# Kernel optimization log

Hardware: AMD Instinct MI355X
Metric: run time of the kernel (lower is better)

## Reference

```python
import jax, jax.numpy as jnp
import numpy as np

STRIDES = (8, 16, 32, 64, 128)
HS = (192, 96, 48, 24, 12)
NUM_CLASSES = 15
NUM_THETA = 18
B = 16
SCORE_THR = 0.05
IOU_THR = 0.3
MAX_DET = 1000


def setup_inputs() -> dict:
    key = jax.random.key(0)
    ks = jax.random.split(key, 20)
    inp = {}
    i = 0
    for name, c in (("cls", NUM_CLASSES), ("reg", 5), ("tc", NUM_THETA), ("tr", 1)):
        for l, h in enumerate(HS):
            inp[f"{name}_l{l}"] = jax.random.normal(ks[i], (B, c, h, h), dtype=jnp.float32)
            i += 1
    return inp


def _coords():
    # FCOS-style location centers per level, concatenated: [N, 2] (x, y)
    outs = []
    for h, s in zip(HS, STRIDES):
        c1d = jnp.arange(h, dtype=jnp.float32) * s + s // 2
        yy, xx = jnp.meshgrid(c1d, c1d, indexing="ij")
        outs.append(jnp.stack([xx.ravel(), yy.ravel()], axis=-1))
    return jnp.concatenate(outs, axis=0)


def _flatten(levels):
    # list of [B,C,h,w] -> [B, sum(h*w), C]  (permute to NHWC then reshape, as in torch)
    b = levels[0].shape[0]
    return jnp.concatenate(
        [jnp.transpose(t, (0, 2, 3, 1)).reshape(b, -1, t.shape[1]) for t in levels], axis=1
    )


def _pairwise_iou(boxes):
    # boxes [M,5] (x1,y1,x2,y2,theta); axis-aligned IoU on first 4 coords
    x1, y1, x2, y2 = boxes[:, 0], boxes[:, 1], boxes[:, 2], boxes[:, 3]
    area = jnp.clip(x2 - x1, 0.0) * jnp.clip(y2 - y1, 0.0)
    iw = jnp.clip(jnp.minimum(x2[:, None], x2[None, :]) - jnp.maximum(x1[:, None], x1[None, :]), 0.0)
    ih = jnp.clip(jnp.minimum(y2[:, None], y2[None, :]) - jnp.maximum(y1[:, None], y1[None, :]), 0.0)
    inter = iw * ih
    union = area[:, None] + area[None, :] - inter
    return inter / jnp.maximum(union, 1e-8)


def _nms_keep(boxes, valid, iou_thr):
    # greedy NMS over score-sorted boxes; returns bool keep mask [M]
    m = boxes.shape[0]
    iou = _pairwise_iou(boxes)
    idx = jnp.arange(m)

    def body(i, keep):
        sup = keep[i] & (iou[i] > iou_thr) & (idx > i)
        return keep & ~sup

    return jax.lax.fori_loop(0, m, body, valid)


def _forward(cls_levels, reg_levels, tc_levels, tr_levels):
    coords = _coords()  # [N,2]

    cls_preds = jax.nn.sigmoid(_flatten(cls_levels))          # [B,N,15]
    cls_scores = jnp.max(cls_preds, axis=-1)                   # [B,N]
    cls_classes = jnp.argmax(cls_preds, axis=-1) + 1           # [B,N]

    tc_preds = jax.nn.sigmoid(_flatten(tc_levels))             # [B,N,18]
    theta_c = (jnp.argmax(tc_preds, axis=-1) + 1)[..., None].astype(jnp.float32)  # [B,N,1]
    tr_lo = _flatten(tr_levels)                                # [B,N,1]
    theta = theta_c * 10.0 + tr_lo                             # [B,N,1]

    # reg: scale ltrb channels (0:4) by stride per level, keep angle channel raw
    reg_parts = []
    for t, s in zip(reg_levels, STRIDES):
        r = jnp.transpose(t, (0, 2, 3, 1)).reshape(t.shape[0], -1, 5)
        reg_parts.append(jnp.concatenate([r[..., :4] * float(s), r[..., 4:]], axis=-1))
    reg = jnp.concatenate(reg_parts, axis=1)                   # [B,N,5]

    x1y1 = coords[None, :, :] - reg[..., :2]
    x2y2 = coords[None, :, :] + reg[..., 2:4]
    boxes = jnp.concatenate([x1y1, x2y2, theta], axis=-1)      # [B,N,5]

    max_num = min(MAX_DET, cls_scores.shape[-1])
    top_scores, top_idx = jax.lax.top_k(cls_scores, max_num)   # sorted desc
    boxes_topk = jnp.take_along_axis(boxes, top_idx[..., None], axis=1)   # [B,M,5]
    classes_topk = jnp.take_along_axis(cls_classes, top_idx, axis=1)      # [B,M]

    valid = top_scores >= SCORE_THR
    keep = jax.vmap(lambda b, v: _nms_keep(b, v, IOU_THR))(boxes_topk, valid)  # [B,M] bool

    scores_post = top_scores * keep
    classes_post = classes_topk * keep
    boxes_post = boxes_topk * keep[..., None]
    return scores_post, classes_post, boxes_post


def reference(cls_l0, cls_l1, cls_l2, cls_l3, cls_l4,
              reg_l0, reg_l1, reg_l2, reg_l3, reg_l4,
              tc_l0, tc_l1, tc_l2, tc_l3, tc_l4,
              tr_l0, tr_l1, tr_l2, tr_l3, tr_l4):
    return _forward(
        [cls_l0, cls_l1, cls_l2, cls_l3, cls_l4],
        [reg_l0, reg_l1, reg_l2, reg_l3, reg_l4],
        [tc_l0, tc_l1, tc_l2, tc_l3, tc_l4],
        [tr_l0, tr_l1, tr_l2, tr_l3, tr_l4],
    )
```

## Files before the change

kernel.cpp:

```cpp
#include <hip/hip_runtime.h>
#include <stdint.h>

#define NCLS   15
#define NTH    18
#define BATCH  16
#define NANCH  49104
#define KTOP   1000
#define NWORDS 16
#define NBIN   32768
#define BSHIFT 15
#define CAND   2048

__device__ __forceinline__ float sigmoidf(float x) {
    return 1.0f / (1.0f + expf(-x));
}

__device__ __forceinline__ void levelOf(int i, int& lvl, int& h, int& s, int& pos) {
    if (i < 36864)      { lvl = 0; h = 192; s = 8;   pos = i; }
    else if (i < 46080) { lvl = 1; h = 96;  s = 16;  pos = i - 36864; }
    else if (i < 48384) { lvl = 2; h = 48;  s = 32;  pos = i - 46080; }
    else if (i < 48960) { lvl = 3; h = 24;  s = 64;  pos = i - 48384; }
    else                { lvl = 4; h = 12;  s = 128; pos = i - 48960; }
}

__device__ __forceinline__ unsigned long long shfl_u64(unsigned long long v, int src) {
    int lo = __shfl((int)(unsigned int)(v & 0xFFFFFFFFull), src);
    int hi = __shfl((int)(unsigned int)(v >> 32), src);
    return ((unsigned long long)(unsigned int)hi << 32) | (unsigned long long)(unsigned int)lo;
}

__device__ __forceinline__ void atomicOr64Shared(unsigned long long* p, unsigned long long v) {
    unsigned int* q = (unsigned int*)p;
    unsigned int lo = (unsigned int)v;
    unsigned int hi = (unsigned int)(v >> 32);
    if (lo) atomicOr(q, lo);
    if (hi) atomicOr(q + 1, hi);
}

__global__ __launch_bounds__(256) void k_zero(uint4* __restrict__ p, int n4)
{
    int i = blockIdx.x * 256 + threadIdx.x;
    if (i < n4) p[i] = make_uint4(0u, 0u, 0u, 0u);
}

__global__ __launch_bounds__(256) void k_scores(
    const float* __restrict__ c0, const float* __restrict__ c1,
    const float* __restrict__ c2, const float* __restrict__ c3,
    const float* __restrict__ c4,
    float* __restrict__ scores, unsigned int* __restrict__ hist)
{
    __shared__ unsigned int lh[NBIN / 2];
    const int b = blockIdx.y;
    for (int i = threadIdx.x; i < NBIN / 2; i += 256) lh[i] = 0u;
    __syncthreads();

    #pragma unroll
    for (int r = 0; r < 2; ++r) {
        int f4 = blockIdx.x * 512 + r * 256 + threadIdx.x;
        if (f4 < NANCH / 4) {
            int i = f4 * 4;
            int lvl, h, s, pos;
            levelOf(i, lvl, h, s, pos);
            int hh = h * h;
            const float* cp = (lvl == 0) ? c0 : (lvl == 1) ? c1 : (lvl == 2) ? c2
                              : (lvl == 3) ? c3 : c4;
            const float* base = cp + (size_t)b * NCLS * hh + pos;
            float4 mx = make_float4(-1e30f, -1e30f, -1e30f, -1e30f);
            #pragma unroll
            for (int c = 0; c < NCLS; ++c) {
                float4 v = *(const float4*)(base + (size_t)c * hh);
                mx.x = fmaxf(mx.x, v.x); mx.y = fmaxf(mx.y, v.y);
                mx.z = fmaxf(mx.z, v.z); mx.w = fmaxf(mx.w, v.w);
            }
            float4 sc = make_float4(sigmoidf(mx.x), sigmoidf(mx.y),
                                    sigmoidf(mx.z), sigmoidf(mx.w));
            *(float4*)(scores + (size_t)b * NANCH + i) = sc;
            unsigned int bin;
            bin = __float_as_uint(sc.x) >> BSHIFT;
            atomicAdd(&lh[bin >> 1], 1u << ((bin & 1) << 4));
            bin = __float_as_uint(sc.y) >> BSHIFT;
            atomicAdd(&lh[bin >> 1], 1u << ((bin & 1) << 4));
            bin = __float_as_uint(sc.z) >> BSHIFT;
            atomicAdd(&lh[bin >> 1], 1u << ((bin & 1) << 4));
            bin = __float_as_uint(sc.w) >> BSHIFT;
            atomicAdd(&lh[bin >> 1], 1u << ((bin & 1) << 4));
        }
    }
    __syncthreads();

    unsigned int* hb = hist + (size_t)b * NBIN;
    for (int wd = threadIdx.x; wd < NBIN / 2; wd += 256) {
        unsigned int v = lh[wd];
        if (v) {
            unsigned int lo = v & 0xFFFFu, hi = v >> 16;
            if (lo) atomicAdd(&hb[wd * 2], lo);
            if (hi) atomicAdd(&hb[wd * 2 + 1], hi);
        }
    }
}

__global__ __launch_bounds__(256) void k_findT(
    const unsigned int* __restrict__ hist, int* __restrict__ tbin)
{
    int b = blockIdx.x;
    int tid = threadIdx.x;
    const unsigned int* hb = hist + (size_t)b * NBIN;
    __shared__ unsigned int sc[256];
    __shared__ unsigned int fsc[128];
    __shared__ int s_c, s_t;

    unsigned int s = 0;
    const uint4* hv = (const uint4*)(hb + (size_t)tid * 128);
    #pragma unroll 8
    for (int k = 0; k < 32; ++k) {
        uint4 v = hv[k];
        s += v.x + v.y + v.z + v.w;
    }
    sc[tid] = s;
    if (tid == 0) { s_c = 0; s_t = 0; }
    __syncthreads();
    for (int d = 1; d < 256; d <<= 1) {
        unsigned int add = (tid + d < 256) ? sc[tid + d] : 0;
        __syncthreads();
        sc[tid] += add;
        __syncthreads();
    }
    if (sc[tid] >= (unsigned int)KTOP && (tid == 255 || sc[tid + 1] < (unsigned int)KTOP))
        s_c = tid;
    __syncthreads();
    int c = s_c;
    unsigned int hi = (c < 255) ? sc[c + 1] : 0;
    if (tid < 128) fsc[tid] = hb[c * 128 + tid];
    __syncthreads();
    for (int d = 1; d < 128; d <<= 1) {
        unsigned int add = (tid < 128 && tid + d < 128) ? fsc[tid + d] : 0;
        __syncthreads();
        if (tid < 128) fsc[tid] += add;
        __syncthreads();
    }
    if (tid < 128 && hi + fsc[tid] >= (unsigned int)KTOP &&
        (tid == 127 || hi + fsc[tid + 1] < (unsigned int)KTOP))
        s_t = tid;
    __syncthreads();
    if (tid == 0) tbin[b] = c * 128 + s_t;
}

__global__ __launch_bounds__(256) void k_compact(
    const float* __restrict__ scores, const int* __restrict__ tbin,
    int* __restrict__ cnt, unsigned long long* __restrict__ cand)
{
    const int b = blockIdx.y;
    const int t4 = blockIdx.x * 256 + threadIdx.x;
    __shared__ int lcnt;
    __shared__ int lbase;
    if (threadIdx.x == 0) lcnt = 0;
    __syncthreads();

    const int T = tbin[b];
    const bool in = (t4 < NANCH / 4);
    float4 v = make_float4(0.f, 0.f, 0.f, 0.f);
    if (in) v = *(const float4*)(scores + (size_t)b * NANCH + 4 * (size_t)t4);
    unsigned int bits[4] = { __float_as_uint(v.x), __float_as_uint(v.y),
                             __float_as_uint(v.z), __float_as_uint(v.w) };
    int rank[4];
    #pragma unroll
    for (int k = 0; k < 4; ++k) {
        bool pass = in && ((int)(bits[k] >> BSHIFT) >= T);
        rank[k] = pass ? atomicAdd(&lcnt, 1) : -1;
    }
    __syncthreads();
    if (threadIdx.x == 0) lbase = atomicAdd(&cnt[b * 16], lcnt);
    __syncthreads();
    const int base = lbase;
    #pragma unroll
    for (int k = 0; k < 4; ++k) {
        if (rank[k] >= 0) {
            int p = base + rank[k];
            if (p < CAND) {
                unsigned int idx = 4u * (unsigned int)t4 + (unsigned int)k;
                cand[(size_t)b * CAND + p] =
                    ((unsigned long long)bits[k] << 32) |
                    (unsigned long long)(0xFFFFFFFFu - idx);
            }
        }
    }
}

__global__ __launch_bounds__(1024) void k_sortk(
    const unsigned long long* __restrict__ cand, const int* __restrict__ cnt,
    float* __restrict__ tsc, int* __restrict__ tix)
{
    int b = blockIdx.x;
    int tid = threadIdx.x;
    __shared__ unsigned long long keys[CAND];
    int n = cnt[b * 16]; if (n > CAND) n = CAND;
    for (int i = tid; i < CAND; i += 1024)
        keys[i] = (i < n) ? cand[(size_t)b * CAND + i] : 0ull;
    __syncthreads();
    for (int sz = 2; sz <= CAND; sz <<= 1) {
        for (int st = sz >> 1; st > 0; st >>= 1) {
            for (int i = tid; i < CAND; i += 1024) {
                int j = i ^ st;
                if (j > i) {
                    unsigned long long a = keys[i], c = keys[j];
                    bool desc = ((i & sz) == 0);
                    if (desc ? (a < c) : (a > c)) { keys[i] = c; keys[j] = a; }
                }
            }
            __syncthreads();
        }
    }
    if (tid < KTOP) {
        unsigned long long key = keys[tid];
        tsc[b * KTOP + tid] = __uint_as_float((unsigned int)(key >> 32));
        tix[b * KTOP + tid] = (int)(0xFFFFFFFFu - (unsigned int)(key & 0xFFFFFFFFull));
    }
}

__global__ __launch_bounds__(256) void k_decode(
    const float* __restrict__ c0, const float* __restrict__ c1,
    const float* __restrict__ c2, const float* __restrict__ c3,
    const float* __restrict__ c4,
    const float* __restrict__ r0, const float* __restrict__ r1,
    const float* __restrict__ r2, const float* __restrict__ r3,
    const float* __restrict__ r4,
    const float* __restrict__ t0, const float* __restrict__ t1,
    const float* __restrict__ t2, const float* __restrict__ t3,
    const float* __restrict__ t4,
    const float* __restrict__ q0, const float* __restrict__ q1,
    const float* __restrict__ q2, const float* __restrict__ q3,
    const float* __restrict__ q4,
    const int* __restrict__ tix, float* __restrict__ boxes, int* __restrict__ clstop)
{
    int g = blockIdx.x * 256 + threadIdx.x;
    if (g >= BATCH * KTOP) return;
    int b = g / KTOP;
    int idx = tix[g];
    int lvl, h, s, pos;
    levelOf(idx, lvl, h, s, pos);
    int y = pos / h, x = pos - y * h;
    int hh = h * h;
    const float* cp = (lvl == 0) ? c0 : (lvl == 1) ? c1 : (lvl == 2) ? c2 : (lvl == 3) ? c3 : c4;
    const float* rp = (lvl == 0) ? r0 : (lvl == 1) ? r1 : (lvl == 2) ? r2 : (lvl == 3) ? r3 : r4;
    const float* tp = (lvl == 0) ? t0 : (lvl == 1) ? t1 : (lvl == 2) ? t2 : (lvl == 3) ? t3 : t4;
    const float* qp = (lvl == 0) ? q0 : (lvl == 1) ? q1 : (lvl == 2) ? q2 : (lvl == 3) ? q3 : q4;
    int off = y * h + x;

    const float* cb = cp + (size_t)b * NCLS * hh + off;
    float bestc = -1e30f; int bc = 0;
    #pragma unroll
    for (int c = 0; c < NCLS; ++c) {
        float v = sigmoidf(cb[(size_t)c * hh]);
        if (v > bestc) { bestc = v; bc = c; }
    }
    clstop[g] = bc + 1;

    const float* tb = tp + (size_t)b * NTH * hh + off;
    float best = -1e30f; int bt = 0;
    #pragma unroll
    for (int c = 0; c < NTH; ++c) {
        float v = sigmoidf(tb[(size_t)c * hh]);
        if (v > best) { best = v; bt = c; }
    }
    float theta = (float)(bt + 1) * 10.0f + qp[(size_t)b * hh + off];

    const float* rb = rp + (size_t)b * 5 * hh + off;
    float fs = (float)s;
    float rr0 = rb[0] * fs;
    float rr1 = rb[(size_t)hh] * fs;
    float rr2 = rb[(size_t)2 * hh] * fs;
    float rr3 = rb[(size_t)3 * hh] * fs;
    float cx = (float)(x * s + (s >> 1));
    float cy = (float)(y * s + (s >> 1));
    float* op = boxes + (size_t)g * 5;
    op[0] = cx - rr0;
    op[1] = cy - rr1;
    op[2] = cx + rr2;
    op[3] = cy + rr3;
    op[4] = theta;
}

__global__ __launch_bounds__(256) void k_mask(
    const float* __restrict__ boxes, unsigned long long* __restrict__ mask)
{
    const int b = blockIdx.x;
    const int by = blockIdx.y;
    __shared__ float bx1[1024], by1[1024], bx2[1024], by2[1024], bar[1024];
    for (int r = threadIdx.x; r < 1024; r += 256) {
        float x1 = 0.f, y1 = 0.f, x2 = 0.f, y2 = 0.f;
        if (r < KTOP) {
            const float* p = boxes + ((size_t)(b * KTOP + r)) * 5;
            x1 = p[0]; y1 = p[1]; x2 = p[2]; y2 = p[3];
        }
        bx1[r] = x1; by1[r] = y1; bx2[r] = x2; by2[r] = y2;
        bar[r] = fmaxf(x2 - x1, 0.0f) * fmaxf(y2 - y1, 0.0f);
    }
    __syncthreads();

    const int l  = threadIdx.x & 63;
    const int wv = threadIdx.x >> 6;
    const int i  = (by << 6) + l;
    const float x1 = bx1[i], y1 = by1[i], x2 = bx2[i], y2 = by2[i], ai = bar[i];

    for (int w = by + wv; w < NWORDS; w += 4) {
        const int j0 = w << 6;
        unsigned long long m = 0ull;
        #pragma unroll 8
        for (int jj = 0; jj < 64; ++jj) {
            const int j = j0 + jj;
            float iw = fminf(x2, bx2[j]) - fmaxf(x1, bx1[j]);
            iw = fmaxf(iw, 0.0f);
            float ih = fminf(y2, by2[j]) - fmaxf(y1, by1[j]);
            ih = fmaxf(ih, 0.0f);
            float inter = iw * ih;
            float u = ai + bar[j] - inter;
            float iou = inter / fmaxf(u, 1e-8f);
            unsigned long long bit = (iou > 0.3f && j > i) ? 1ull : 0ull;
            m |= bit << jj;
        }
        mask[(((size_t)b * 1024 + i) << 4) + w] = m;
    }
}

#define LOADROW(R, W) do {                                                          \
    const ulonglong2* rp2 = (const ulonglong2*)(mask +                              \
        (((size_t)b * 1024 + ((W) << 6) + l) << 4));                                \
    _Pragma("unroll")                                                               \
    for (int p = 0; p < 8; ++p) {                                                   \
        ulonglong2 v = rp2[p]; R[2 * p] = v.x; R[2 * p + 1] = v.y;                  \
    }                                                                               \
} while (0)

#define PROC(W, R) do {                                                             \
    const unsigned long long rowword = R[W];                                        \
    unsigned long long zr = __ballot(rowword == 0ull);                              \
    unsigned long long remw = sremv[W];                                             \
    unsigned long long pend = vw[W] & ~remw;                                        \
    unsigned long long keptm = 0ull;                                                \
    while (pend) {                                                                  \
        unsigned long long nzp = pend & ~zr;                                        \
        if (!nzp) { keptm |= pend; break; }                                         \
        int jj = __builtin_ctzll(nzp);                                              \
        unsigned long long low = (1ull << jj); low = (low << 1) - 1ull;             \
        keptm |= pend & low;                                                        \
        remw |= shfl_u64(rowword, jj);                                              \
        pend &= ~low; pend &= ~remw;                                                \
    }                                                                               \
    if (l == 0) skeep[W] = keptm;                                                   \
    if ((keptm >> l) & 1ull) {                                                      \
        _Pragma("unroll")                                                           \
        for (int w2 = (W) + 1; w2 < NWORDS; ++w2)                                   \
            if (R[w2]) atomicOr64Shared(&sremv[w2], R[w2]);                         \
    }                                                                               \
} while (0)

__global__ __launch_bounds__(64) void k_nms(
    const unsigned long long* __restrict__ mask,
    const float* __restrict__ tsc, const int* __restrict__ clstop,
    const float* __restrict__ boxes, float* __restrict__ out)
{
    const int b = blockIdx.x;
    const int l = threadIdx.x;
    __shared__ unsigned long long sremv[NWORDS];
    __shared__ unsigned long long skeep[NWORDS];

    if (l < NWORDS) sremv[l] = 0ull;

    unsigned long long vw[NWORDS];
    #pragma unroll
    for (int w = 0; w < NWORDS; ++w) {
        int i = (w << 6) + l;
        bool v = (i < KTOP) && (tsc[b * KTOP + i] >= 0.05f);
        vw[w] = __ballot(v);
    }

    unsigned long long rowA[NWORDS], rowB[NWORDS];
    LOADROW(rowA, 0);
    LOADROW(rowB, 1);   PROC(0, rowA);
    LOADROW(rowA, 2);   PROC(1, rowB);
    LOADROW(rowB, 3);   PROC(2, rowA);
    LOADROW(rowA, 4);   PROC(3, rowB);
    LOADROW(rowB, 5);   PROC(4, rowA);
    LOADROW(rowA, 6);   PROC(5, rowB);
    LOADROW(rowB, 7);   PROC(6, rowA);
    LOADROW(rowA, 8);   PROC(7, rowB);
    LOADROW(rowB, 9);   PROC(8, rowA);
    LOADROW(rowA, 10);  PROC(9, rowB);
    LOADROW(rowB, 11);  PROC(10, rowA);
    LOADROW(rowA, 12);  PROC(11, rowB);
    LOADROW(rowB, 13);  PROC(12, rowA);
    LOADROW(rowA, 14);  PROC(13, rowB);
    LOADROW(rowB, 15);  PROC(14, rowA);
    PROC(15, rowB);

    #pragma unroll
    for (int w = 0; w < NWORDS; ++w) {
        int i = (w << 6) + l;
        if (i < KTOP) {
            int g = b * KTOP + i;
            float fk = (float)((skeep[w] >> l) & 1ull);
            out[g] = tsc[g] * fk;
            out[BATCH * KTOP + g] = (float)clstop[g] * fk;
            const float* bp = boxes + (size_t)g * 5;
            float* op = out + 2 * BATCH * KTOP + (size_t)g * 5;
            op[0] = bp[0] * fk;
            op[1] = bp[1] * fk;
            op[2] = bp[2] * fk;
            op[3] = bp[3] * fk;
            op[4] = bp[4] * fk;
        }
    }
}

extern "C" void kernel_launch(void* const* d_in, const int* in_sizes, int n_in,
                              void* d_out, int out_size, void* d_ws, size_t ws_size,
                              hipStream_t stream) {
    const float* c0 = (const float*)d_in[0];
    const float* c1 = (const float*)d_in[1];
    const float* c2 = (const float*)d_in[2];
    const float* c3 = (const float*)d_in[3];
    const float* c4 = (const float*)d_in[4];
    const float* r0 = (const float*)d_in[5];
    const float* r1 = (const float*)d_in[6];
    const float* r2 = (const float*)d_in[7];
    const float* r3 = (const float*)d_in[8];
    const float* r4 = (const float*)d_in[9];
    const float* t0 = (const float*)d_in[10];
    const float* t1 = (const float*)d_in[11];
    const float* t2 = (const float*)d_in[12];
    const float* t3 = (const float*)d_in[13];
    const float* t4 = (const float*)d_in[14];
    const float* q0 = (const float*)d_in[15];
    const float* q1 = (const float*)d_in[16];
    const float* q2 = (const float*)d_in[17];
    const float* q3 = (const float*)d_in[18];
    const float* q4 = (const float*)d_in[19];

    char* ws = (char*)d_ws;
    float*              scores  = (float*)(ws + 0);
    float*              tsc     = (float*)(ws + 3142656);
    int*                tix     = (int*)(ws + 3206656);
    float*              boxes   = (float*)(ws + 3270656);
    unsigned long long* cand    = (unsigned long long*)(ws + 3270656);
    int*                clstop  = (int*)(ws + 3590656);
    unsigned long long* mask    = (unsigned long long*)(ws + 3654656);
    unsigned int*       hist    = (unsigned int*)(ws + 3654656);
    int*                tcnt    = (int*)(ws + 5751808);
    int*                tbin    = (int*)(ws + 5752832);
    float*              out     = (float*)d_out;

    const int n4 = 2098176 / 16;
    k_zero<<<(n4 + 255) / 256, 256, 0, stream>>>((uint4*)(ws + 3654656), n4);

    k_scores<<<dim3(24, BATCH), 256, 0, stream>>>(
        c0, c1, c2, c3, c4, scores, hist);
    k_findT<<<BATCH, 256, 0, stream>>>(hist, tbin);
    k_compact<<<dim3(48, BATCH), 256, 0, stream>>>(scores, tbin, tcnt, cand);
    k_sortk<<<BATCH, 1024, 0, stream>>>(cand, tcnt, tsc, tix);
    k_decode<<<(BATCH * KTOP + 255) / 256, 256, 0, stream>>>(
        c0, c1, c2, c3, c4,
        r0, r1, r2, r3, r4, t0, t1, t2, t3, t4, q0, q1, q2, q3, q4,
        tix, boxes, clstop);
    k_mask<<<dim3(BATCH, 16), 256, 0, stream>>>(boxes, mask);
    k_nms<<<BATCH, 64, 0, stream>>>(mask, tsc, clstop, boxes, out);
}
```

Baseline: 122.4 us.

## Replace bitonic top-k sort with rank-by-counting fused into box decode

The per-batch 2048-element bitonic sort in a single 1024-thread block is replaced by a rank-counting kernel. Each thread counts how many candidate keys exceed its own and, if it ranks in the top 1000, decodes its box directly at that rank. This spreads the work over 8x16 blocks and removes a launch plus the tix round-trip through global memory. The cost is O(CAND^2) shared-memory comparisons per batch, and workspace offsets are rearranged so cand no longer aliases boxes.

```diff
diff --git a/kernel.cpp b/kernel.cpp
--- a/kernel.cpp
+++ b/kernel.cpp
@@ -186,38 +186,8 @@
     }
 }
 
-__global__ __launch_bounds__(1024) void k_sortk(
+__global__ __launch_bounds__(256) void k_rankdec(
     const unsigned long long* __restrict__ cand, const int* __restrict__ cnt,
-    float* __restrict__ tsc, int* __restrict__ tix)
-{
-    int b = blockIdx.x;
-    int tid = threadIdx.x;
-    __shared__ unsigned long long keys[CAND];
-    int n = cnt[b * 16]; if (n > CAND) n = CAND;
-    for (int i = tid; i < CAND; i += 1024)
-        keys[i] = (i < n) ? cand[(size_t)b * CAND + i] : 0ull;
-    __syncthreads();
-    for (int sz = 2; sz <= CAND; sz <<= 1) {
-        for (int st = sz >> 1; st > 0; st >>= 1) {
-            for (int i = tid; i < CAND; i += 1024) {
-                int j = i ^ st;
-                if (j > i) {
-                    unsigned long long a = keys[i], c = keys[j];
-                    bool desc = ((i & sz) == 0);
-                    if (desc ? (a < c) : (a > c)) { keys[i] = c; keys[j] = a; }
-                }
-            }
-            __syncthreads();
-        }
-    }
-    if (tid < KTOP) {
-        unsigned long long key = keys[tid];
-        tsc[b * KTOP + tid] = __uint_as_float((unsigned int)(key >> 32));
-        tix[b * KTOP + tid] = (int)(0xFFFFFFFFu - (unsigned int)(key & 0xFFFFFFFFull));
-    }
-}
-
-__global__ __launch_bounds__(256) void k_decode(
     const float* __restrict__ c0, const float* __restrict__ c1,
     const float* __restrict__ c2, const float* __restrict__ c3,
     const float* __restrict__ c4,
@@ -230,12 +200,30 @@
     const float* __restrict__ q0, const float* __restrict__ q1,
     const float* __restrict__ q2, const float* __restrict__ q3,
     const float* __restrict__ q4,
-    const int* __restrict__ tix, float* __restrict__ boxes, int* __restrict__ clstop)
-{
-    int g = blockIdx.x * 256 + threadIdx.x;
-    if (g >= BATCH * KTOP) return;
-    int b = g / KTOP;
-    int idx = tix[g];
+    float* __restrict__ tsc, float* __restrict__ boxes, int* __restrict__ clstop)
+{
+    const int b  = blockIdx.y;
+    const int ci = blockIdx.x * 256 + threadIdx.x;
+    __shared__ unsigned long long keys[CAND];
+
+    int n = cnt[b * 16]; if (n > CAND) n = CAND;
+    for (int i = threadIdx.x; i < CAND; i += 256)
+        keys[i] = (i < n) ? cand[(size_t)b * CAND + i] : 0ull;
+    __syncthreads();
+
+    const unsigned long long my = keys[ci];
+    if (my == 0ull) return;
+
+    int rank = 0;
+    #pragma unroll 8
+    for (int j = 0; j < CAND; ++j)
+        rank += (keys[j] > my) ? 1 : 0;
+    if (rank >= KTOP) return;
+
+    const int g   = b * KTOP + rank;
+    const int idx = (int)(0xFFFFFFFFu - (unsigned int)(my & 0xFFFFFFFFull));
+    tsc[g] = __uint_as_float((unsigned int)(my >> 32));
+
     int lvl, h, s, pos;
     levelOf(idx, lvl, h, s, pos);
     int y = pos / h, x = pos - y * h;
@@ -439,28 +427,27 @@
     char* ws = (char*)d_ws;
     float*              scores  = (float*)(ws + 0);
     float*              tsc     = (float*)(ws + 3142656);
-    int*                tix     = (int*)(ws + 3206656);
+    int*                clstop  = (int*)(ws + 3206656);
     float*              boxes   = (float*)(ws + 3270656);
-    unsigned long long* cand    = (unsigned long long*)(ws + 3270656);
-    int*                clstop  = (int*)(ws + 3590656);
-    unsigned long long* mask    = (unsigned long long*)(ws + 3654656);
-    unsigned int*       hist    = (unsigned int*)(ws + 3654656);
-    int*                tcnt    = (int*)(ws + 5751808);
-    int*                tbin    = (int*)(ws + 5752832);
+    unsigned long long* mask    = (unsigned long long*)(ws + 3590656);
+    unsigned int*       hist    = (unsigned int*)(ws + 3590656);
+    unsigned long long* cand    = (unsigned long long*)(ws + 5687808);
+    int*                tcnt    = (int*)(ws + 5949952);
+    int*                tbin    = (int*)(ws + 5950976);
     float*              out     = (float*)d_out;
 
-    const int n4 = 2098176 / 16;
-    k_zero<<<(n4 + 255) / 256, 256, 0, stream>>>((uint4*)(ws + 3654656), n4);
+    const int n4 = 2360384 / 16;
+    k_zero<<<(n4 + 255) / 256, 256, 0, stream>>>((uint4*)(ws + 3590656), n4);
 
     k_scores<<<dim3(24, BATCH), 256, 0, stream>>>(
         c0, c1, c2, c3, c4, scores, hist);
     k_findT<<<BATCH, 256, 0, stream>>>(hist, tbin);
     k_compact<<<dim3(48, BATCH), 256, 0, stream>>>(scores, tbin, tcnt, cand);
-    k_sortk<<<BATCH, 1024, 0, stream>>>(cand, tcnt, tsc, tix);
-    k_decode<<<(BATCH * KTOP + 255) / 256, 256, 0, stream>>>(
+    k_rankdec<<<dim3(8, BATCH), 256, 0, stream>>>(
+        cand, tcnt,
         c0, c1, c2, c3, c4,
         r0, r1, r2, r3, r4, t0, t1, t2, t3, t4, q0, q1, q2, q3, q4,
-        tix, boxes, clstop);
+        tsc, boxes, clstop);
     k_mask<<<dim3(BATCH, 16), 256, 0, stream>>>(boxes, mask);
     k_nms<<<BATCH, 64, 0, stream>>>(mask, tsc, clstop, boxes, out);
 }
```

New measurement: 122.5 us. Within noise of the previous version (+0.1%).
